# Kernel optimization log

Measured on AMD Instinct MI355X. Metric: run time of the kernel, lower is better.

## Reference

```python
import jax, jax.numpy as jnp
import numpy as np

N = 8192      # nodes
E = 16384     # query edges
D = 256       # node feature dim
NNZ = 262144  # overlap matrix nnz (avg degree 32)
P1, P2, P3 = 32, 32, 32


def _mlp(x, W1, b1, W2, b2):
    # Linear(1->p) -> ReLU -> Linear(p->1)
    return jax.nn.relu(x @ W1 + b1) @ W2 + b2


def setup_inputs() -> dict:
    key = jax.random.key(0)
    ks = jax.random.split(key, 16)
    inp = {
        "edges": jax.random.randint(ks[0], (E, 2), 0, N, dtype=jnp.int32),
        "row": jax.random.randint(ks[1], (NNZ,), 0, N, dtype=jnp.int32),
        "col": jax.random.randint(ks[2], (NNZ,), 0, N, dtype=jnp.int32),
        "values": jax.random.uniform(ks[3], (NNZ,), dtype=jnp.float32),
        "H": jax.random.normal(ks[4], (N, D), dtype=jnp.float32),
        # f_edge: 1 -> P1 -> 1
        "we1": jax.random.normal(ks[5], (1, P1), dtype=jnp.float32) * 0.5,
        "be1": jnp.zeros((P1,), jnp.float32),
        "we2": jax.random.normal(ks[6], (P1, 1), dtype=jnp.float32) * 0.5,
        "be2": jnp.zeros((1,), jnp.float32),
        # f_node: 1 -> P2 -> 1
        "wn1": jax.random.normal(ks[7], (1, P2), dtype=jnp.float32) * 0.5,
        "bn1": jnp.zeros((P2,), jnp.float32),
        "wn2": jax.random.normal(ks[8], (P2, 1), dtype=jnp.float32) * 0.5,
        "bn2": jnp.zeros((1,), jnp.float32),
        # psi_3: 1 -> P3 -> 1
        "wp1": jax.random.normal(ks[9], (1, P3), dtype=jnp.float32) * 0.5,
        "bp1": jnp.zeros((P3,), jnp.float32),
        "wp2": jax.random.normal(ks[10], (P3, 1), dtype=jnp.float32) * 0.5,
        "bp2": jnp.zeros((1,), jnp.float32),
        "alpha": jnp.zeros((2,), jnp.float32),
    }
    return inp


def reference(edges, row, col, values, H,
              we1, be1, we2, be2,
              wn1, bn1, wn2, bn2,
              wp1, bp1, wp2, bp2, alpha):
    src, dst = edges[:, 0], edges[:, 1]

    # --- BatchDotPred: sigmoid(<H[src], H[dst]>) ---
    h_link = jax.nn.sigmoid(jnp.einsum('ed,ed->e', H[src], H[dst]))[:, None]  # [E,1]

    # --- MultiHopAggregator ---
    edge_feat = _mlp(values[:, None], we1, be1, we2, be2)           # [NNZ,1]
    node_in = jax.ops.segment_sum(edge_feat, col, num_segments=N)  # [N,1] scatter_add over col
    struct = _mlp(node_in, wn1, bn1, wn2, bn2)[:, 0]                # [N]

    # dense overlap adjacency (coo.todense(), duplicates summed)
    adj = jnp.zeros((N, N), values.dtype).at[row, col].add(values)  # [N,N]

    # NOTE: faithful to source bug: both src and dst neighborhoods gather src rows
    sn = adj[src]                                                   # [E,N]
    agg = jnp.einsum('en,n->e', sn * sn, struct * struct)[:, None]  # [E,1]

    z_link = jax.nn.sigmoid(_mlp(agg, wp1, bp1, wp2, bp2))          # [E,1]

    a = jax.nn.softmax(alpha)
    y_hat = a[0] * z_link + a[1] * h_link + 1e-15
    return y_hat
```

## Files before the change

### kernel.cpp

```cpp
#include <hip/hip_runtime.h>
#include <math.h>

#define N_NODES 8192
#define D_DIM   256
#define E_EDGES 16384
#define NNZ_CNT 262144

#define NBLK 64
#define BTHR 1024
#define PER_BLK (NNZ_CNT / NBLK)
#define NODES_PER_BLK (N_NODES / NBLK)

__device__ unsigned g_arrive = 0;
__device__ unsigned g_depart = 0;

__device__ __forceinline__ void st_agent(float* p, float v) {
    __hip_atomic_store(p, v, __ATOMIC_RELAXED, __HIP_MEMORY_SCOPE_AGENT);
}
__device__ __forceinline__ float ld_agent(const float* p) {
    return __hip_atomic_load(p, __ATOMIC_RELAXED, __HIP_MEMORY_SCOPE_AGENT);
}

__device__ __forceinline__ void sw_barrier(unsigned target) {
    __syncthreads();
    if (threadIdx.x == 0) {
        __hip_atomic_fetch_add(&g_arrive, 1u, __ATOMIC_RELAXED,
                               __HIP_MEMORY_SCOPE_AGENT);
        while (__hip_atomic_load(&g_arrive, __ATOMIC_RELAXED,
                                 __HIP_MEMORY_SCOPE_AGENT) < target)
            __builtin_amdgcn_s_sleep(1);
    }
    __syncthreads();
}

__device__ __forceinline__ float sigmoidf(float x) {
    return 1.0f / (1.0f + expf(-x));
}

struct Params {
    const int*   edges;
    const int*   row;
    const int*   col;
    const float* values;
    const float* H;
    const float* we1; const float* be1; const float* we2; const float* be2;
    const float* wn1; const float* bn1; const float* wn2; const float* bn2;
    const float* wp1; const float* bp1; const float* wp2; const float* bp2;
    const float* alpha;
    float* out;
    float* partA;
    float* partB;
    float* struct2;
    float* znode;
};

__global__ __launch_bounds__(BTHR) void k_fused(Params p) {
    __shared__ float bins[N_NODES];
    __shared__ float s2[N_NODES];
    const int tid  = threadIdx.x;
    const int bid  = blockIdx.x;
    const int base = bid * PER_BLK;

    for (int j = tid; j < N_NODES; j += BTHR) bins[j] = 0.0f;
    __syncthreads();
#pragma unroll
    for (int it = 0; it < PER_BLK / BTHR; ++it) {
        int k = base + it * BTHR + tid;
        float v = p.values[k];
        int c = p.col[k];
        float f = p.be2[0];
#pragma unroll
        for (int j = 0; j < 32; ++j) {
            float t = fmaf(v, p.we1[j], p.be1[j]);
            t = t > 0.0f ? t : 0.0f;
            f = fmaf(t, p.we2[j], f);
        }
        atomicAdd(&bins[c], f);
    }
    __syncthreads();
    {
        float* pa = p.partA + (size_t)bid * N_NODES;
        for (int j = tid; j < N_NODES; j += BTHR) st_agent(&pa[j], bins[j]);
    }
    sw_barrier(1 * NBLK);

    if (tid < NODES_PER_BLK) {
        int node = bid * NODES_PER_BLK + tid;
        float x = 0.0f;
#pragma unroll 8
        for (int b = 0; b < NBLK; ++b)
            x += ld_agent(&p.partA[(size_t)b * N_NODES + node]);
        float u = p.bn2[0];
#pragma unroll
        for (int j = 0; j < 32; ++j) {
            float t = fmaf(x, p.wn1[j], p.bn1[j]);
            t = t > 0.0f ? t : 0.0f;
            u = fmaf(t, p.wn2[j], u);
        }
        st_agent(&p.struct2[node], u * u);
    }
    sw_barrier(2 * NBLK);

    for (int j = tid; j < N_NODES; j += BTHR) {
        bins[j] = 0.0f;
        s2[j] = ld_agent(&p.struct2[j]);
    }
    __syncthreads();
#pragma unroll
    for (int it = 0; it < PER_BLK / BTHR; ++it) {
        int k = base + it * BTHR + tid;
        float v = p.values[k];
        int r = p.row[k];
        int c = p.col[k];
        atomicAdd(&bins[r], v * v * s2[c]);
    }
    __syncthreads();
    {
        float* pb = p.partB + (size_t)bid * N_NODES;
        for (int j = tid; j < N_NODES; j += BTHR) st_agent(&pb[j], bins[j]);
    }
    sw_barrier(3 * NBLK);

    if (tid < NODES_PER_BLK) {
        int node = bid * NODES_PER_BLK + tid;
        float x = 0.0f;
#pragma unroll 8
        for (int b = 0; b < NBLK; ++b)
            x += ld_agent(&p.partB[(size_t)b * N_NODES + node]);
        float u = p.bp2[0];
#pragma unroll
        for (int j = 0; j < 32; ++j) {
            float t = fmaf(x, p.wp1[j], p.bp1[j]);
            t = t > 0.0f ? t : 0.0f;
            u = fmaf(t, p.wp2[j], u);
        }
        st_agent(&p.znode[node], sigmoidf(u));
    }
    sw_barrier(4 * NBLK);

    {
        const int wave  = (bid * BTHR + tid) >> 6;
        const int lane  = tid & 63;
        const int nwave = (NBLK * BTHR) >> 6;
        float m  = fmaxf(p.alpha[0], p.alpha[1]);
        float e0 = expf(p.alpha[0] - m);
        float e1 = expf(p.alpha[1] - m);
        float inv = 1.0f / (e0 + e1);
        float a0 = e0 * inv, a1 = e1 * inv;
        const float4* H4 = (const float4*)p.H;
        for (int e = wave; e < E_EDGES; e += nwave) {
            int src = p.edges[2 * e];
            int dst = p.edges[2 * e + 1];
            float4 a4 = H4[src * (D_DIM / 4) + lane];
            float4 b4 = H4[dst * (D_DIM / 4) + lane];
            float dot = a4.x * b4.x + a4.y * b4.y + a4.z * b4.z + a4.w * b4.w;
#pragma unroll
            for (int off = 32; off >= 1; off >>= 1)
                dot += __shfl_xor(dot, off, 64);
            if (lane == 0) {
                float h = sigmoidf(dot);
                float z = ld_agent(&p.znode[src]);
                p.out[e] = a0 * z + a1 * h + 1e-15f;
            }
        }
    }

    if (tid == 0) {
        unsigned old = __hip_atomic_fetch_add(&g_depart, 1u, __ATOMIC_RELAXED,
                                              __HIP_MEMORY_SCOPE_AGENT);
        if (old == NBLK - 1) {
            __hip_atomic_store(&g_arrive, 0u, __ATOMIC_RELAXED,
                               __HIP_MEMORY_SCOPE_AGENT);
            __hip_atomic_store(&g_depart, 0u, __ATOMIC_RELAXED,
                               __HIP_MEMORY_SCOPE_AGENT);
        }
    }
}

extern "C" void kernel_launch(void* const* d_in, const int* in_sizes, int n_in,
                              void* d_out, int out_size, void* d_ws, size_t ws_size,
                              hipStream_t stream) {
    Params prm;
    prm.edges  = (const int*)d_in[0];
    prm.row    = (const int*)d_in[1];
    prm.col    = (const int*)d_in[2];
    prm.values = (const float*)d_in[3];
    prm.H      = (const float*)d_in[4];
    prm.we1 = (const float*)d_in[5];  prm.be1 = (const float*)d_in[6];
    prm.we2 = (const float*)d_in[7];  prm.be2 = (const float*)d_in[8];
    prm.wn1 = (const float*)d_in[9];  prm.bn1 = (const float*)d_in[10];
    prm.wn2 = (const float*)d_in[11]; prm.bn2 = (const float*)d_in[12];
    prm.wp1 = (const float*)d_in[13]; prm.bp1 = (const float*)d_in[14];
    prm.wp2 = (const float*)d_in[15]; prm.bp2 = (const float*)d_in[16];
    prm.alpha = (const float*)d_in[17];
    prm.out = (float*)d_out;

    float* ws_f = (float*)d_ws;
    prm.partA   = ws_f;
    prm.partB   = ws_f + (size_t)NBLK * N_NODES;
    prm.struct2 = ws_f + (size_t)2 * NBLK * N_NODES;
    prm.znode   = prm.struct2 + N_NODES;

    k_fused<<<dim3(NBLK), dim3(BTHR), 0, stream>>>(prm);
}
```

Before: 145.4 us.

## Hoist H dot products before barriers, parallelize partial reductions, use flag barrier

Moves the H[src]·H[dst] dot-product phase to the start of the kernel so its memory traffic happens before the synchronized sparse phases, stores the sigmoid results to a workspace buffer, and finishes with a cheap per-edge combine. The cross-block partial-sum reductions now use all 1024 threads (8 partial slices each plus a shared-memory combine) instead of 128 threads each serially loading 64 values. The counter-based grid barrier becomes a per-phase flag barrier in which block 0 polls all flags and releases the others. This adds an extra global write and read of the edge results, and a reset loop over the flags at kernel end.

New measurement: 158.1 us. +8.7%, slower.

```diff
diff --git a/kernel.cpp b/kernel.cpp
--- a/kernel.cpp
+++ b/kernel.cpp
@@ -11,7 +11,8 @@
 #define PER_BLK (NNZ_CNT / NBLK)
 #define NODES_PER_BLK (N_NODES / NBLK)
 
-__device__ unsigned g_arrive = 0;
+__device__ unsigned g_flags[4][NBLK];
+__device__ unsigned g_release[4];
 __device__ unsigned g_depart = 0;
 
 __device__ __forceinline__ void st_agent(float* p, float v) {
@@ -20,15 +21,26 @@
 __device__ __forceinline__ float ld_agent(const float* p) {
     return __hip_atomic_load(p, __ATOMIC_RELAXED, __HIP_MEMORY_SCOPE_AGENT);
 }
-
-__device__ __forceinline__ void sw_barrier(unsigned target) {
-    __syncthreads();
-    if (threadIdx.x == 0) {
-        __hip_atomic_fetch_add(&g_arrive, 1u, __ATOMIC_RELAXED,
-                               __HIP_MEMORY_SCOPE_AGENT);
-        while (__hip_atomic_load(&g_arrive, __ATOMIC_RELAXED,
-                                 __HIP_MEMORY_SCOPE_AGENT) < target)
-            __builtin_amdgcn_s_sleep(1);
+__device__ __forceinline__ void st_agent_u(unsigned* p, unsigned v) {
+    __hip_atomic_store(p, v, __ATOMIC_RELAXED, __HIP_MEMORY_SCOPE_AGENT);
+}
+__device__ __forceinline__ unsigned ld_agent_u(const unsigned* p) {
+    return __hip_atomic_load(p, __ATOMIC_RELAXED, __HIP_MEMORY_SCOPE_AGENT);
+}
+
+__device__ __forceinline__ void sw_barrier(int phase) {
+    __syncthreads();
+    const int tid = threadIdx.x, bid = blockIdx.x;
+    if (tid < 64) {
+        if (tid == 0) st_agent_u(&g_flags[phase][bid], 1u);
+        if (bid == 0) {
+            while (ld_agent_u(&g_flags[phase][tid]) == 0)
+                __builtin_amdgcn_s_sleep(1);
+            if (tid == 0) st_agent_u(&g_release[phase], 1u);
+        } else if (tid == 0) {
+            while (ld_agent_u(&g_release[phase]) == 0)
+                __builtin_amdgcn_s_sleep(1);
+        }
     }
     __syncthreads();
 }
@@ -52,6 +64,7 @@
     float* partB;
     float* struct2;
     float* znode;
+    float* hbuf;
 };
 
 __global__ __launch_bounds__(BTHR) void k_fused(Params p) {
@@ -63,90 +76,11 @@
 
     for (int j = tid; j < N_NODES; j += BTHR) bins[j] = 0.0f;
     __syncthreads();
-#pragma unroll
-    for (int it = 0; it < PER_BLK / BTHR; ++it) {
-        int k = base + it * BTHR + tid;
-        float v = p.values[k];
-        int c = p.col[k];
-        float f = p.be2[0];
-#pragma unroll
-        for (int j = 0; j < 32; ++j) {
-            float t = fmaf(v, p.we1[j], p.be1[j]);
-            t = t > 0.0f ? t : 0.0f;
-            f = fmaf(t, p.we2[j], f);
-        }
-        atomicAdd(&bins[c], f);
-    }
-    __syncthreads();
-    {
-        float* pa = p.partA + (size_t)bid * N_NODES;
-        for (int j = tid; j < N_NODES; j += BTHR) st_agent(&pa[j], bins[j]);
-    }
-    sw_barrier(1 * NBLK);
-
-    if (tid < NODES_PER_BLK) {
-        int node = bid * NODES_PER_BLK + tid;
-        float x = 0.0f;
-#pragma unroll 8
-        for (int b = 0; b < NBLK; ++b)
-            x += ld_agent(&p.partA[(size_t)b * N_NODES + node]);
-        float u = p.bn2[0];
-#pragma unroll
-        for (int j = 0; j < 32; ++j) {
-            float t = fmaf(x, p.wn1[j], p.bn1[j]);
-            t = t > 0.0f ? t : 0.0f;
-            u = fmaf(t, p.wn2[j], u);
-        }
-        st_agent(&p.struct2[node], u * u);
-    }
-    sw_barrier(2 * NBLK);
-
-    for (int j = tid; j < N_NODES; j += BTHR) {
-        bins[j] = 0.0f;
-        s2[j] = ld_agent(&p.struct2[j]);
-    }
-    __syncthreads();
-#pragma unroll
-    for (int it = 0; it < PER_BLK / BTHR; ++it) {
-        int k = base + it * BTHR + tid;
-        float v = p.values[k];
-        int r = p.row[k];
-        int c = p.col[k];
-        atomicAdd(&bins[r], v * v * s2[c]);
-    }
-    __syncthreads();
-    {
-        float* pb = p.partB + (size_t)bid * N_NODES;
-        for (int j = tid; j < N_NODES; j += BTHR) st_agent(&pb[j], bins[j]);
-    }
-    sw_barrier(3 * NBLK);
-
-    if (tid < NODES_PER_BLK) {
-        int node = bid * NODES_PER_BLK + tid;
-        float x = 0.0f;
-#pragma unroll 8
-        for (int b = 0; b < NBLK; ++b)
-            x += ld_agent(&p.partB[(size_t)b * N_NODES + node]);
-        float u = p.bp2[0];
-#pragma unroll
-        for (int j = 0; j < 32; ++j) {
-            float t = fmaf(x, p.wp1[j], p.bp1[j]);
-            t = t > 0.0f ? t : 0.0f;
-            u = fmaf(t, p.wp2[j], u);
-        }
-        st_agent(&p.znode[node], sigmoidf(u));
-    }
-    sw_barrier(4 * NBLK);
 
     {
         const int wave  = (bid * BTHR + tid) >> 6;
         const int lane  = tid & 63;
         const int nwave = (NBLK * BTHR) >> 6;
-        float m  = fmaxf(p.alpha[0], p.alpha[1]);
-        float e0 = expf(p.alpha[0] - m);
-        float e1 = expf(p.alpha[1] - m);
-        float inv = 1.0f / (e0 + e1);
-        float a0 = e0 * inv, a1 = e1 * inv;
         const float4* H4 = (const float4*)p.H;
         for (int e = wave; e < E_EDGES; e += nwave) {
             int src = p.edges[2 * e];
@@ -157,11 +91,111 @@
 #pragma unroll
             for (int off = 32; off >= 1; off >>= 1)
                 dot += __shfl_xor(dot, off, 64);
-            if (lane == 0) {
-                float h = sigmoidf(dot);
-                float z = ld_agent(&p.znode[src]);
-                p.out[e] = a0 * z + a1 * h + 1e-15f;
+            if (lane == 0) st_agent(&p.hbuf[e], sigmoidf(dot));
+        }
+    }
+
+#pragma unroll
+    for (int it = 0; it < PER_BLK / BTHR; ++it) {
+        int k = base + it * BTHR + tid;
+        float v = p.values[k];
+        int c = p.col[k];
+        float f = p.be2[0];
+#pragma unroll
+        for (int j = 0; j < 32; ++j) {
+            float t = fmaf(v, p.we1[j], p.be1[j]);
+            t = t > 0.0f ? t : 0.0f;
+            f = fmaf(t, p.we2[j], f);
+        }
+        atomicAdd(&bins[c], f);
+    }
+    __syncthreads();
+    {
+        float* pa = p.partA + (size_t)bid * N_NODES;
+        for (int j = tid; j < N_NODES; j += BTHR) st_agent(&pa[j], bins[j]);
+    }
+    sw_barrier(0);
+
+    {
+        int node = bid * NODES_PER_BLK + (tid & 127);
+        int b0   = (tid >> 7) * 8;
+        float x = 0.0f;
+#pragma unroll
+        for (int i = 0; i < 8; ++i)
+            x += ld_agent(&p.partA[(size_t)(b0 + i) * N_NODES + node]);
+        s2[tid] = x;
+        __syncthreads();
+        if (tid < NODES_PER_BLK) {
+            float xx = 0.0f;
+#pragma unroll
+            for (int i = 0; i < 8; ++i) xx += s2[tid + 128 * i];
+            float u = p.bn2[0];
+#pragma unroll
+            for (int j = 0; j < 32; ++j) {
+                float t = fmaf(xx, p.wn1[j], p.bn1[j]);
+                t = t > 0.0f ? t : 0.0f;
+                u = fmaf(t, p.wn2[j], u);
             }
+            st_agent(&p.struct2[bid * NODES_PER_BLK + tid], u * u);
+        }
+        __syncthreads();
+        for (int j = tid; j < N_NODES; j += BTHR) bins[j] = 0.0f;
+    }
+    sw_barrier(1);
+
+    for (int j = tid; j < N_NODES; j += BTHR) s2[j] = ld_agent(&p.struct2[j]);
+    __syncthreads();
+#pragma unroll
+    for (int it = 0; it < PER_BLK / BTHR; ++it) {
+        int k = base + it * BTHR + tid;
+        float v = p.values[k];
+        int r = p.row[k];
+        int c = p.col[k];
+        atomicAdd(&bins[r], v * v * s2[c]);
+    }
+    __syncthreads();
+    {
+        float* pb = p.partB + (size_t)bid * N_NODES;
+        for (int j = tid; j < N_NODES; j += BTHR) st_agent(&pb[j], bins[j]);
+    }
+    sw_barrier(2);
+
+    {
+        int node = bid * NODES_PER_BLK + (tid & 127);
+        int b0   = (tid >> 7) * 8;
+        float x = 0.0f;
+#pragma unroll
+        for (int i = 0; i < 8; ++i)
+            x += ld_agent(&p.partB[(size_t)(b0 + i) * N_NODES + node]);
+        bins[tid] = x;
+        __syncthreads();
+        if (tid < NODES_PER_BLK) {
+            float xx = 0.0f;
+#pragma unroll
+            for (int i = 0; i < 8; ++i) xx += bins[tid + 128 * i];
+            float u = p.bp2[0];
+#pragma unroll
+            for (int j = 0; j < 32; ++j) {
+                float t = fmaf(xx, p.wp1[j], p.bp1[j]);
+                t = t > 0.0f ? t : 0.0f;
+                u = fmaf(t, p.wp2[j], u);
+            }
+            st_agent(&p.znode[bid * NODES_PER_BLK + tid], sigmoidf(u));
+        }
+    }
+    sw_barrier(3);
+
+    {
+        int gid = bid * BTHR + tid;
+        if (gid < E_EDGES) {
+            float m  = fmaxf(p.alpha[0], p.alpha[1]);
+            float e0 = expf(p.alpha[0] - m);
+            float e1 = expf(p.alpha[1] - m);
+            float inv = 1.0f / (e0 + e1);
+            int src = p.edges[2 * gid];
+            float z = ld_agent(&p.znode[src]);
+            float h = ld_agent(&p.hbuf[gid]);
+            p.out[gid] = (e0 * inv) * z + (e1 * inv) * h + 1e-15f;
         }
     }
 
@@ -169,10 +203,11 @@
         unsigned old = __hip_atomic_fetch_add(&g_depart, 1u, __ATOMIC_RELAXED,
                                               __HIP_MEMORY_SCOPE_AGENT);
         if (old == NBLK - 1) {
-            __hip_atomic_store(&g_arrive, 0u, __ATOMIC_RELAXED,
-                               __HIP_MEMORY_SCOPE_AGENT);
-            __hip_atomic_store(&g_depart, 0u, __ATOMIC_RELAXED,
-                               __HIP_MEMORY_SCOPE_AGENT);
+            for (int ph = 0; ph < 4; ++ph) {
+                st_agent_u(&g_release[ph], 0u);
+                for (int b = 0; b < NBLK; ++b) st_agent_u(&g_flags[ph][b], 0u);
+            }
+            st_agent_u(&g_depart, 0u);
         }
     }
 }
@@ -200,6 +235,7 @@
     prm.partB   = ws_f + (size_t)NBLK * N_NODES;
     prm.struct2 = ws_f + (size_t)2 * NBLK * N_NODES;
     prm.znode   = prm.struct2 + N_NODES;
+    prm.hbuf    = prm.znode + N_NODES;
 
     k_fused<<<dim3(NBLK), dim3(BTHR), 0, stream>>>(prm);
 }
```

## Hoist edge dot products before first barrier and parallelize partial reductions

Applied to the files above, without the earlier changes.

Moves the H[src]·H[dst] dot-product computation to the start of the kernel, before the first grid barrier, and stores the per-edge sigmoid in shared memory. The final phase then only gathers znode and writes the output. The irregular H gathers can overlap with the scatter phase, and load imbalance at the barriers shrinks. The cross-block partial-sum reductions now use all 1024 threads, each summing 8 of the 64 partials, followed by a shared-memory combine, instead of 128 threads each doing 64 serial loads. The bins reset is also moved ahead of the second barrier.

After: 134.0 us. -7.8%, faster.

```diff
diff --git a/kernel.cpp b/kernel.cpp
--- a/kernel.cpp
+++ b/kernel.cpp
@@ -10,6 +10,7 @@
 #define BTHR 1024
 #define PER_BLK (NNZ_CNT / NBLK)
 #define NODES_PER_BLK (N_NODES / NBLK)
+#define EDGES_PER_BLK (E_EDGES / NBLK)
 
 __device__ unsigned g_arrive = 0;
 __device__ unsigned g_depart = 0;
@@ -57,12 +58,34 @@
 __global__ __launch_bounds__(BTHR) void k_fused(Params p) {
     __shared__ float bins[N_NODES];
     __shared__ float s2[N_NODES];
+    __shared__ float hl[EDGES_PER_BLK];
     const int tid  = threadIdx.x;
     const int bid  = blockIdx.x;
     const int base = bid * PER_BLK;
 
     for (int j = tid; j < N_NODES; j += BTHR) bins[j] = 0.0f;
     __syncthreads();
+
+    {
+        const int w    = tid >> 6;
+        const int lane = tid & 63;
+        const float4* H4 = (const float4*)p.H;
+#pragma unroll
+        for (int i = 0; i < EDGES_PER_BLK / 16; ++i) {
+            int le = w * 16 + i;
+            int e  = bid * EDGES_PER_BLK + le;
+            int src = p.edges[2 * e];
+            int dst = p.edges[2 * e + 1];
+            float4 a4 = H4[src * (D_DIM / 4) + lane];
+            float4 b4 = H4[dst * (D_DIM / 4) + lane];
+            float dot = a4.x * b4.x + a4.y * b4.y + a4.z * b4.z + a4.w * b4.w;
+#pragma unroll
+            for (int off = 32; off >= 1; off >>= 1)
+                dot += __shfl_xor(dot, off, 64);
+            if (lane == 0) hl[le] = sigmoidf(dot);
+        }
+    }
+
 #pragma unroll
     for (int it = 0; it < PER_BLK / BTHR; ++it) {
         int k = base + it * BTHR + tid;
@@ -84,27 +107,34 @@
     }
     sw_barrier(1 * NBLK);
 
-    if (tid < NODES_PER_BLK) {
-        int node = bid * NODES_PER_BLK + tid;
+    {
+        int node = bid * NODES_PER_BLK + (tid & 127);
+        int b0   = (tid >> 7) * 8;
         float x = 0.0f;
-#pragma unroll 8
-        for (int b = 0; b < NBLK; ++b)
-            x += ld_agent(&p.partA[(size_t)b * N_NODES + node]);
-        float u = p.bn2[0];
-#pragma unroll
-        for (int j = 0; j < 32; ++j) {
-            float t = fmaf(x, p.wn1[j], p.bn1[j]);
-            t = t > 0.0f ? t : 0.0f;
-            u = fmaf(t, p.wn2[j], u);
-        }
-        st_agent(&p.struct2[node], u * u);
+#pragma unroll
+        for (int i = 0; i < 8; ++i)
+            x += ld_agent(&p.partA[(size_t)(b0 + i) * N_NODES + node]);
+        s2[tid] = x;
+        __syncthreads();
+        if (tid < NODES_PER_BLK) {
+            float xx = 0.0f;
+#pragma unroll
+            for (int i = 0; i < 8; ++i) xx += s2[tid + 128 * i];
+            float u = p.bn2[0];
+#pragma unroll
+            for (int j = 0; j < 32; ++j) {
+                float t = fmaf(xx, p.wn1[j], p.bn1[j]);
+                t = t > 0.0f ? t : 0.0f;
+                u = fmaf(t, p.wn2[j], u);
+            }
+            st_agent(&p.struct2[bid * NODES_PER_BLK + tid], u * u);
+        }
+        __syncthreads();
+        for (int j = tid; j < N_NODES; j += BTHR) bins[j] = 0.0f;
     }
     sw_barrier(2 * NBLK);
 
-    for (int j = tid; j < N_NODES; j += BTHR) {
-        bins[j] = 0.0f;
-        s2[j] = ld_agent(&p.struct2[j]);
-    }
+    for (int j = tid; j < N_NODES; j += BTHR) s2[j] = ld_agent(&p.struct2[j]);
     __syncthreads();
 #pragma unroll
     for (int it = 0; it < PER_BLK / BTHR; ++it) {
@@ -121,48 +151,40 @@
     }
     sw_barrier(3 * NBLK);
 
-    if (tid < NODES_PER_BLK) {
-        int node = bid * NODES_PER_BLK + tid;
+    {
+        int node = bid * NODES_PER_BLK + (tid & 127);
+        int b0   = (tid >> 7) * 8;
         float x = 0.0f;
-#pragma unroll 8
-        for (int b = 0; b < NBLK; ++b)
-            x += ld_agent(&p.partB[(size_t)b * N_NODES + node]);
-        float u = p.bp2[0];
-#pragma unroll
-        for (int j = 0; j < 32; ++j) {
-            float t = fmaf(x, p.wp1[j], p.bp1[j]);
-            t = t > 0.0f ? t : 0.0f;
-            u = fmaf(t, p.wp2[j], u);
-        }
-        st_agent(&p.znode[node], sigmoidf(u));
+#pragma unroll
+        for (int i = 0; i < 8; ++i)
+            x += ld_agent(&p.partB[(size_t)(b0 + i) * N_NODES + node]);
+        bins[tid] = x;
+        __syncthreads();
+        if (tid < NODES_PER_BLK) {
+            float xx = 0.0f;
+#pragma unroll
+            for (int i = 0; i < 8; ++i) xx += bins[tid + 128 * i];
+            float u = p.bp2[0];
+#pragma unroll
+            for (int j = 0; j < 32; ++j) {
+                float t = fmaf(xx, p.wp1[j], p.bp1[j]);
+                t = t > 0.0f ? t : 0.0f;
+                u = fmaf(t, p.wp2[j], u);
+            }
+            st_agent(&p.znode[bid * NODES_PER_BLK + tid], sigmoidf(u));
+        }
     }
     sw_barrier(4 * NBLK);
 
-    {
-        const int wave  = (bid * BTHR + tid) >> 6;
-        const int lane  = tid & 63;
-        const int nwave = (NBLK * BTHR) >> 6;
+    if (tid < EDGES_PER_BLK) {
+        int e = bid * EDGES_PER_BLK + tid;
         float m  = fmaxf(p.alpha[0], p.alpha[1]);
         float e0 = expf(p.alpha[0] - m);
         float e1 = expf(p.alpha[1] - m);
         float inv = 1.0f / (e0 + e1);
-        float a0 = e0 * inv, a1 = e1 * inv;
-        const float4* H4 = (const float4*)p.H;
-        for (int e = wave; e < E_EDGES; e += nwave) {
-            int src = p.edges[2 * e];
-            int dst = p.edges[2 * e + 1];
-            float4 a4 = H4[src * (D_DIM / 4) + lane];
-            float4 b4 = H4[dst * (D_DIM / 4) + lane];
-            float dot = a4.x * b4.x + a4.y * b4.y + a4.z * b4.z + a4.w * b4.w;
-#pragma unroll
-            for (int off = 32; off >= 1; off >>= 1)
-                dot += __shfl_xor(dot, off, 64);
-            if (lane == 0) {
-                float h = sigmoidf(dot);
-                float z = ld_agent(&p.znode[src]);
-                p.out[e] = a0 * z + a1 * h + 1e-15f;
-            }
-        }
+        int src = p.edges[2 * e];
+        float z = ld_agent(&p.znode[src]);
+        p.out[e] = (e0 * inv) * z + (e1 * inv) * hl[tid] + 1e-15f;
     }
 
     if (tid == 0) {
```
